# Performance work log

Hardware: AMD Instinct MI355X
Metric: run time of the kernel (lower is better)

## Reference

```python
import jax, jax.numpy as jnp
import numpy as np

N = 100000       # nodes
E = 1600000      # edges (avg degree 16)
F_IN = 20        # NUM_FEATURES
H = 128          # hidden_channels
EPS = 1e-5       # GraphNorm eps


def setup_inputs() -> dict:
    key = jax.random.key(0)
    ks = jax.random.split(key, 24)
    s = 0.05
    inp = {
        "x": jax.random.normal(ks[0], (N, F_IN), jnp.float32),
        "edge_index": jax.random.randint(ks[1], (2, E), 0, N, dtype=jnp.int32),
    }
    # SAGEConv params: lin_l (neighbors, with bias), lin_r (root, no bias)
    dims = [(F_IN, H), (H, H), (H, H)]
    k = 2
    for i, (din, dout) in enumerate(dims):
        inp[f"Wl{i}"] = jax.random.normal(ks[k], (dout, din), jnp.float32) * s; k += 1
        inp[f"bl{i}"] = jnp.zeros((dout,), jnp.float32)
        inp[f"Wr{i}"] = jax.random.normal(ks[k], (dout, din), jnp.float32) * s; k += 1
        # GraphNorm: weight, bias, mean_scale (alpha)
        inp[f"gw{i}"] = jnp.ones((dout,), jnp.float32)
        inp[f"gb{i}"] = jnp.zeros((dout,), jnp.float32)
        inp[f"ga{i}"] = jnp.ones((dout,), jnp.float32)
    # MLP head: 128 -> 64 -> 32 -> 1
    inp["hW1"] = jax.random.normal(ks[k], (64, H), jnp.float32) * s; k += 1
    inp["hb1"] = jnp.zeros((64,), jnp.float32)
    inp["hW2"] = jax.random.normal(ks[k], (32, 64), jnp.float32) * s; k += 1
    inp["hb2"] = jnp.zeros((32,), jnp.float32)
    inp["hW3"] = jax.random.normal(ks[k], (1, 32), jnp.float32) * s; k += 1
    inp["hb3"] = jnp.zeros((1,), jnp.float32)
    return inp


def _sage(x, src, dst, Wl, bl, Wr):
    # mean aggregation of source features at destination nodes
    deg = jax.ops.segment_sum(jnp.ones((src.shape[0],), x.dtype), dst, num_segments=N)
    agg = jax.ops.segment_sum(x[src], dst, num_segments=N)
    agg = agg / jnp.maximum(deg, 1.0)[:, None]
    return agg @ Wl.T + bl + x @ Wr.T


def _graphnorm(x, w, b, a):
    # single graph (batch=None): stats over all nodes, per channel
    mean = jnp.mean(x, axis=0)
    c = x - a * mean
    var = jnp.mean(c * c, axis=0)
    return w * c * jax.lax.rsqrt(var + EPS) + b


def reference(x, edge_index,
              Wl0, bl0, Wr0, gw0, gb0, ga0,
              Wl1, bl1, Wr1, gw1, gb1, ga1,
              Wl2, bl2, Wr2, gw2, gb2, ga2,
              hW1, hb1, hW2, hb2, hW3, hb3):
    src, dst = edge_index[0], edge_index[1]
    layers = [(Wl0, bl0, Wr0, gw0, gb0, ga0),
              (Wl1, bl1, Wr1, gw1, gb1, ga1),
              (Wl2, bl2, Wr2, gw2, gb2, ga2)]
    h = x
    for (Wl, bl, Wr, gw, gb, ga) in layers:
        h = _sage(h, src, dst, Wl, bl, Wr)
        h = _graphnorm(h, gw, gb, ga)
        h = jax.nn.gelu(h, approximate=False)  # dropout: eval mode (identity)
    h = jax.nn.gelu(h @ hW1.T + hb1, approximate=False)
    h = jax.nn.gelu(h @ hW2.T + hb2, approximate=False)
    out = jax.nn.sigmoid(h @ hW3.T + hb3)
    return out.squeeze(-1)  # [N]
```

## Files before the change

kernel.cpp:

```cpp
#include <hip/hip_runtime.h>
#include <hip/hip_bf16.h>
#include <math.h>

#define NN 100000
#define EE 1600000
#define FIN 20
#define HH 128
#define NBUK 391
#define FILLB 196
#define MMB 782

typedef __attribute__((ext_vector_type(8))) short bf16x8;
typedef __attribute__((ext_vector_type(4))) float f32x4;

__device__ __forceinline__ unsigned short f2b(float x) {
    unsigned int b = __float_as_uint(x);
    unsigned int r = b + 0x7fffu + ((b >> 16) & 1u);
    return (unsigned short)(r >> 16);
}
__device__ __forceinline__ float lof(unsigned int u) { return __uint_as_float(u << 16); }
__device__ __forceinline__ float hif(unsigned int u) { return __uint_as_float(u & 0xffff0000u); }

__device__ __forceinline__ float gelu_exact(float z) {
    return 0.5f * z * (1.0f + erff(z * 0.70710678118654752f));
}

__global__ __launch_bounds__(256) void kb_cnt(const int* __restrict__ dst,
                                              int* __restrict__ bcnt) {
    __shared__ int c[NBUK];
    int t = threadIdx.x;
    for (int i = t; i < NBUK; i += 256) c[i] = 0;
    __syncthreads();
    int e0 = blockIdx.x * 8192;
    #pragma unroll 4
    for (int i = 0; i < 32; ++i) {
        int e = e0 + i * 256 + t;
        if (e < EE) atomicAdd(&c[dst[e] >> 8], 1);
    }
    __syncthreads();
    for (int i = t; i < NBUK; i += 256) if (c[i]) atomicAdd(&bcnt[i], c[i]);
}

__global__ void kb_scan(const int* __restrict__ bcnt, int* __restrict__ bbase,
                        int* __restrict__ cursor) {
    __shared__ int sh[512];
    int t = threadIdx.x;
    int v = (t < NBUK) ? bcnt[t] : 0;
    sh[t] = v;
    __syncthreads();
    for (int off = 1; off < 512; off <<= 1) {
        int add = (t >= off) ? sh[t - off] : 0;
        __syncthreads();
        sh[t] += add;
        __syncthreads();
    }
    if (t < NBUK) {
        int ex = sh[t] - v;
        bbase[t] = ex;
        cursor[t] = ex;
    }
    if (t == NBUK - 1) bbase[NBUK] = sh[t];
}

__global__ __launch_bounds__(256) void kb_fill(const int* __restrict__ src,
        const int* __restrict__ dst, int* __restrict__ cursor,
        unsigned int* __restrict__ pairs) {
    __shared__ int cnt[NBUK], base[NBUK], boff[NBUK];
    int t = threadIdx.x;
    for (int i = t; i < NBUK; i += 256) { cnt[i] = 0; boff[i] = 0; }
    __syncthreads();
    int e0 = blockIdx.x * 8192;
    #pragma unroll 4
    for (int i = 0; i < 32; ++i) {
        int e = e0 + i * 256 + t;
        if (e < EE) atomicAdd(&cnt[dst[e] >> 8], 1);
    }
    __syncthreads();
    for (int i = t; i < NBUK; i += 256)
        if (cnt[i]) base[i] = atomicAdd(&cursor[i], cnt[i]);
    __syncthreads();
    #pragma unroll 4
    for (int i = 0; i < 32; ++i) {
        int e = e0 + i * 256 + t;
        if (e < EE) {
            int d = dst[e];
            int b = d >> 8;
            int pos = base[b] + atomicAdd(&boff[b], 1);
            pairs[pos] = (unsigned int)src[e] | ((unsigned int)(d & 255) << 17);
        }
    }
}

__global__ __launch_bounds__(256) void kb_csr(const unsigned int* __restrict__ pairs,
        const int* __restrict__ bbase, int* __restrict__ row_start,
        int* __restrict__ deg, float* __restrict__ invdeg, int* __restrict__ col) {
    __shared__ int ldeg[256];
    __shared__ int lcnt[256];
    int b = blockIdx.x, t = threadIdx.x;
    int e0 = bbase[b], e1 = bbase[b + 1];
    ldeg[t] = 0;
    lcnt[t] = 0;
    __syncthreads();
    for (int e = e0 + t; e < e1; e += 256) atomicAdd(&ldeg[pairs[e] >> 17], 1);
    __syncthreads();
    int d = ldeg[t];
    for (int off = 1; off < 256; off <<= 1) {
        int add = (t >= off) ? ldeg[t - off] : 0;
        __syncthreads();
        ldeg[t] += add;
        __syncthreads();
    }
    int n = b * 256 + t;
    if (n < NN) {
        row_start[n] = e0 + ldeg[t] - d;
        deg[n] = d;
        invdeg[n] = 1.0f / fmaxf((float)d, 1.0f);
    }
    __syncthreads();
    for (int e = e0 + t; e < e1; e += 256) {
        unsigned int p = pairs[e];
        int dL = p >> 17;
        int pos = e0 + (dL ? ldeg[dL - 1] : 0) + atomicAdd(&lcnt[dL], 1);
        col[pos] = (int)(p & 0x1FFFFu);
    }
}

__global__ __launch_bounds__(256) void k_packx(const float* __restrict__ x,
        unsigned short* __restrict__ A0) {
    int id = blockIdx.x * 256 + threadIdx.x;
    int n = id >> 6, k = id & 63;
    if (n >= NN) return;
    if (k < FIN) return;
    float v = (k >= 32 && k < 32 + FIN) ? x[n * FIN + (k - 32)] : 0.0f;
    A0[id] = f2b(v);
}

__global__ void k_agg0(const float* __restrict__ x, const int* __restrict__ rs,
                       const int* __restrict__ deg, const float* __restrict__ inv,
                       const int* __restrict__ col, unsigned short* __restrict__ A0) {
    int g = threadIdx.x >> 5;
    int l = threadIdx.x & 31;
    int n = blockIdx.x * 4 + g;
    if (n >= NN || l >= FIN) return;
    int s = rs[n], d = deg[n];
    float acc = 0.0f;
    int j = 0;
    for (; j + 1 < d; j += 2) {
        int c0 = col[s + j], c1 = col[s + j + 1];
        acc += x[c0 * FIN + l] + x[c1 * FIN + l];
    }
    if (j < d) acc += x[col[s + j] * FIN + l];
    A0[(size_t)n * 64 + l] = f2b(acc * inv[n]);
}

__global__ void k_pack0(const float* __restrict__ Wl, const float* __restrict__ Wr,
                        unsigned short* __restrict__ Wt) {
    int id = blockIdx.x * 256 + threadIdx.x;
    int c = id >> 6, k = id & 63;
    float v = 0.0f;
    if (k < FIN) v = Wl[c * FIN + k];
    else if (k >= 32 && k < 32 + FIN) v = Wr[c * FIN + (k - 32)];
    Wt[id] = f2b(v);
}

__global__ __launch_bounds__(64) void k_aggb(const unsigned short* __restrict__ hB,
        const int* __restrict__ rs, const int* __restrict__ deg,
        const float* __restrict__ inv, const int* __restrict__ col,
        unsigned short* __restrict__ aggB) {
    int n = blockIdx.x;
    int t = threadIdx.x;
    int s = rs[n], d = deg[n];
    const unsigned int* h32 = (const unsigned int*)hB;
    float a0 = 0.0f, a1 = 0.0f;
    int j = 0;
    for (; j + 3 < d; j += 4) {
        int c0 = col[s + j], c1 = col[s + j + 1];
        int c2 = col[s + j + 2], c3 = col[s + j + 3];
        unsigned int u0 = h32[(size_t)c0 * 64 + t];
        unsigned int u1 = h32[(size_t)c1 * 64 + t];
        unsigned int u2 = h32[(size_t)c2 * 64 + t];
        unsigned int u3 = h32[(size_t)c3 * 64 + t];
        a0 += lof(u0) + lof(u1) + lof(u2) + lof(u3);
        a1 += hif(u0) + hif(u1) + hif(u2) + hif(u3);
    }
    for (; j < d; ++j) {
        unsigned int u = h32[(size_t)col[s + j] * 64 + t];
        a0 += lof(u);
        a1 += hif(u);
    }
    float iv = inv[n];
    unsigned int o = (unsigned int)f2b(a0 * iv) | ((unsigned int)f2b(a1 * iv) << 16);
    ((unsigned int*)aggB)[(size_t)n * 64 + t] = o;
}

__global__ void k_pack_main(const float* __restrict__ Wl, const float* __restrict__ Wr,
                            unsigned short* __restrict__ Wt) {
    int id = blockIdx.x * 256 + threadIdx.x;
    int c = id >> 8, k = id & 255;
    float v = (k < HH) ? Wl[c * HH + k] : Wr[c * HH + (k - HH)];
    Wt[id] = f2b(v);
}

__global__ void k_pack_head(const float* __restrict__ hW1, const float* __restrict__ hW2,
                            const float* __restrict__ hb1, const float* __restrict__ hb2,
                            unsigned short* __restrict__ W1b, unsigned short* __restrict__ W2b,
                            float* __restrict__ bH1, float* __restrict__ bH2) {
    int id = blockIdx.x * 256 + threadIdx.x;
    if (id < 16384) {
        int c = id >> 7, k = id & 127;
        W1b[id] = f2b((c < 64) ? hW1[c * 128 + k] : 0.0f);
    } else if (id < 16384 + 2048) {
        int i = id - 16384;
        W2b[i] = f2b(hW2[i]);
    } else if (id < 16384 + 2048 + 128) {
        int i = id - 16384 - 2048;
        bH1[i] = (i < 64) ? hb1[i] : 0.0f;
    } else if (id < 16384 + 2048 + 160) {
        int i = id - 16384 - 2048 - 128;
        bH2[i] = hb2[i];
    }
}

__global__ __launch_bounds__(256) void k_mm(const unsigned short* __restrict__ A0,
        const unsigned short* __restrict__ A1, int c0, int kChunks, int lda,
        const unsigned short* __restrict__ B, int ldb,
        const float* __restrict__ bias, unsigned short* __restrict__ outB,
        float* __restrict__ psPart, float* __restrict__ pqPart, int M) {
    __shared__ __align__(16) unsigned short As[128 * 40];
    __shared__ __align__(16) unsigned short Bs[128 * 40];
    __shared__ float redS[2][128], redQ[2][128];
    const int tid = threadIdx.x;
    const int m0 = blockIdx.x * 128;
    const int w = tid >> 6, lane = tid & 63;
    const int wr = w >> 1, wc = w & 1;
    const int m16 = lane & 15, q = lane >> 4;

    f32x4 acc[4][4];
    #pragma unroll
    for (int i = 0; i < 4; ++i)
        #pragma unroll
        for (int j = 0; j < 4; ++j) acc[i][j] = (f32x4){0.f, 0.f, 0.f, 0.f};

    for (int chunk = 0; chunk < kChunks; ++chunk) {
        const unsigned short* A = (chunk < c0) ? A0 : A1;
        const int kb = (chunk - ((chunk < c0) ? 0 : c0)) * 32;
        #pragma unroll
        for (int it = 0; it < 2; ++it) {
            int s = tid + it * 256;
            int r = s >> 2, p = s & 3;
            int gm = m0 + r;
            uint4 v = make_uint4(0u, 0u, 0u, 0u);
            if (gm < M) v = *(const uint4*)(A + (size_t)gm * lda + kb + p * 8);
            *(uint4*)&As[r * 40 + p * 8] = v;
        }
        {
            const int kbB = chunk * 32;
            #pragma unroll
            for (int it = 0; it < 2; ++it) {
                int s = tid + it * 256;
                int r = s >> 2, p = s & 3;
                uint4 v = *(const uint4*)(B + (size_t)r * ldb + kbB + p * 8);
                *(uint4*)&Bs[r * 40 + p * 8] = v;
            }
        }
        __syncthreads();
        bf16x8 af[4], bfr[4];
        #pragma unroll
        for (int i = 0; i < 4; ++i)
            af[i] = *(const bf16x8*)&As[(wr * 64 + i * 16 + m16) * 40 + q * 8];
        #pragma unroll
        for (int j = 0; j < 4; ++j)
            bfr[j] = *(const bf16x8*)&Bs[(wc * 64 + j * 16 + m16) * 40 + q * 8];
        #pragma unroll
        for (int i = 0; i < 4; ++i)
            #pragma unroll
            for (int j = 0; j < 4; ++j)
                acc[i][j] = __builtin_amdgcn_mfma_f32_16x16x32_bf16(af[i], bfr[j], acc[i][j], 0, 0, 0);
        __syncthreads();
    }

    float cs[4] = {0.f, 0.f, 0.f, 0.f};
    float cq[4] = {0.f, 0.f, 0.f, 0.f};
    #pragma unroll
    for (int i = 0; i < 4; ++i) {
        int mBase = m0 + wr * 64 + i * 16 + q * 4;
        #pragma unroll
        for (int j = 0; j < 4; ++j) {
            int cc = wc * 64 + j * 16 + m16;
            float bv = bias[cc];
            #pragma unroll
            for (int r = 0; r < 4; ++r) {
                int m = mBase + r;
                float v = (m < M) ? (acc[i][j][r] + bv) : 0.0f;
                if (m < M) outB[(size_t)m * 128 + cc] = f2b(v);
                cs[j] += v;
                cq[j] += v * v;
            }
        }
    }
    #pragma unroll
    for (int msk = 16; msk < 64; msk <<= 1) {
        #pragma unroll
        for (int j = 0; j < 4; ++j) {
            cs[j] += __shfl_xor(cs[j], msk, 64);
            cq[j] += __shfl_xor(cq[j], msk, 64);
        }
    }
    if (q == 0) {
        #pragma unroll
        for (int j = 0; j < 4; ++j) {
            int cc = wc * 64 + j * 16 + m16;
            redS[wr][cc] = cs[j];
            redQ[wr][cc] = cq[j];
        }
    }
    __syncthreads();
    if (tid < 128) {
        psPart[(size_t)blockIdx.x * 128 + tid] = redS[0][tid] + redS[1][tid];
        pqPart[(size_t)blockIdx.x * 128 + tid] = redQ[0][tid] + redQ[1][tid];
    }
}

__global__ __launch_bounds__(1024) void k_gn_final(const float* __restrict__ ps,
        const float* __restrict__ pq, const float* __restrict__ gw,
        const float* __restrict__ gb, const float* __restrict__ ga,
        float* __restrict__ cA, float* __restrict__ cB, int nP) {
    __shared__ float shs[8][128], shq[8][128];
    int c = threadIdx.x & 127, sl = threadIdx.x >> 7;
    float s = 0.0f, q = 0.0f;
    for (int b = sl; b < nP; b += 8) {
        s += ps[b * 128 + c];
        q += pq[b * 128 + c];
    }
    shs[sl][c] = s;
    shq[sl][c] = q;
    __syncthreads();
    if (threadIdx.x < 128) {
        float S = 0.0f, Q = 0.0f;
        #pragma unroll
        for (int i = 0; i < 8; ++i) { S += shs[i][c]; Q += shq[i][c]; }
        float mean = S / (float)NN;
        float msq  = Q / (float)NN;
        float a = ga[c];
        float var = msq - mean * mean * a * (2.0f - a);
        float rstd = rsqrtf(var + 1e-5f);
        float A = gw[c] * rstd;
        cA[c] = A;
        cB[c] = gb[c] - a * mean * A;
    }
}

__global__ __launch_bounds__(256) void k_gn_apply(const unsigned short* __restrict__ yB,
        const float* __restrict__ cA, const float* __restrict__ cB,
        unsigned short* __restrict__ hB) {
    int i = blockIdx.x * 256 + threadIdx.x;
    if (i >= NN * 16) return;
    int g = i & 15;
    uint4 v = ((const uint4*)yB)[i];
    float4 A0 = ((const float4*)cA)[g * 2];
    float4 A1 = ((const float4*)cA)[g * 2 + 1];
    float4 B0 = ((const float4*)cB)[g * 2];
    float4 B1 = ((const float4*)cB)[g * 2 + 1];
    unsigned int o0 = (unsigned int)f2b(gelu_exact(lof(v.x) * A0.x + B0.x))
                    | ((unsigned int)f2b(gelu_exact(hif(v.x) * A0.y + B0.y)) << 16);
    unsigned int o1 = (unsigned int)f2b(gelu_exact(lof(v.y) * A0.z + B0.z))
                    | ((unsigned int)f2b(gelu_exact(hif(v.y) * A0.w + B0.w)) << 16);
    unsigned int o2 = (unsigned int)f2b(gelu_exact(lof(v.z) * A1.x + B1.x))
                    | ((unsigned int)f2b(gelu_exact(hif(v.z) * A1.y + B1.y)) << 16);
    unsigned int o3 = (unsigned int)f2b(gelu_exact(lof(v.w) * A1.z + B1.z))
                    | ((unsigned int)f2b(gelu_exact(hif(v.w) * A1.w + B1.w)) << 16);
    ((uint4*)hB)[i] = make_uint4(o0, o1, o2, o3);
}

__global__ __launch_bounds__(256) void k_headf(const unsigned short* __restrict__ hB,
        const unsigned short* __restrict__ W1b, const float* __restrict__ b1,
        const unsigned short* __restrict__ W2b, const float* __restrict__ b2,
        const float* __restrict__ W3, const float* __restrict__ b3,
        float* __restrict__ out) {
    __shared__ __align__(16) unsigned short As[128 * 40];
    __shared__ __align__(16) unsigned short Bs[128 * 40];
    __shared__ __align__(16) unsigned short As2[128 * 72];
    __shared__ __align__(16) unsigned short Bs2[32 * 72];
    const int tid = threadIdx.x;
    const int m0 = blockIdx.x * 128;
    const int w = tid >> 6, lane = tid & 63;
    const int wr = w >> 1, wc = w & 1;
    const int m16 = lane & 15, q = lane >> 4;

    f32x4 acc1[4][4];
    #pragma unroll
    for (int i = 0; i < 4; ++i)
        #pragma unroll
        for (int j = 0; j < 4; ++j) acc1[i][j] = (f32x4){0.f, 0.f, 0.f, 0.f};

    for (int chunk = 0; chunk < 4; ++chunk) {
        const int kb = chunk * 32;
        #pragma unroll
        for (int it = 0; it < 2; ++it) {
            int s = tid + it * 256;
            int r = s >> 2, p = s & 3;
            int gm = m0 + r;
            uint4 v = make_uint4(0u, 0u, 0u, 0u);
            if (gm < NN) v = *(const uint4*)(hB + (size_t)gm * 128 + kb + p * 8);
            *(uint4*)&As[r * 40 + p * 8] = v;
        }
        #pragma unroll
        for (int it = 0; it < 2; ++it) {
            int s = tid + it * 256;
            int r = s >> 2, p = s & 3;
            uint4 v = *(const uint4*)(W1b + (size_t)r * 128 + kb + p * 8);
            *(uint4*)&Bs[r * 40 + p * 8] = v;
        }
        __syncthreads();
        bf16x8 af[4], bfr[4];
        #pragma unroll
        for (int i = 0; i < 4; ++i)
            af[i] = *(const bf16x8*)&As[(wr * 64 + i * 16 + m16) * 40 + q * 8];
        #pragma unroll
        for (int j = 0; j < 4; ++j)
            bfr[j] = *(const bf16x8*)&Bs[(wc * 64 + j * 16 + m16) * 40 + q * 8];
        #pragma unroll
        for (int i = 0; i < 4; ++i)
            #pragma unroll
            for (int j = 0; j < 4; ++j)
                acc1[i][j] = __builtin_amdgcn_mfma_f32_16x16x32_bf16(af[i], bfr[j], acc1[i][j], 0, 0, 0);
        __syncthreads();
    }

    #pragma unroll
    for (int it = 0; it < 8; ++it) {
        int i = tid + it * 256;
        if (i < 2048) Bs2[(i >> 6) * 72 + (i & 63)] = W2b[i];
    }
    if (wc == 0) {
        float b1v[4];
        #pragma unroll
        for (int j = 0; j < 4; ++j) b1v[j] = b1[j * 16 + m16];
        #pragma unroll
        for (int i = 0; i < 4; ++i) {
            int mloc = wr * 64 + i * 16 + q * 4;
            #pragma unroll
            for (int j = 0; j < 4; ++j) {
                int c = j * 16 + m16;
                #pragma unroll
                for (int r = 0; r < 4; ++r)
                    As2[(mloc + r) * 72 + c] = f2b(gelu_exact(acc1[i][j][r] + b1v[j]));
            }
        }
    }
    __syncthreads();

    f32x4 acc2[2][2];
    #pragma unroll
    for (int i = 0; i < 2; ++i)
        #pragma unroll
        for (int j = 0; j < 2; ++j) acc2[i][j] = (f32x4){0.f, 0.f, 0.f, 0.f};
    #pragma unroll
    for (int kc = 0; kc < 2; ++kc) {
        bf16x8 a2[2], bf2[2];
        #pragma unroll
        for (int i = 0; i < 2; ++i)
            a2[i] = *(const bf16x8*)&As2[(w * 32 + i * 16 + m16) * 72 + kc * 32 + q * 8];
        #pragma unroll
        for (int j = 0; j < 2; ++j)
            bf2[j] = *(const bf16x8*)&Bs2[(j * 16 + m16) * 72 + kc * 32 + q * 8];
        #pragma unroll
        for (int i = 0; i < 2; ++i)
            #pragma unroll
            for (int j = 0; j < 2; ++j)
                acc2[i][j] = __builtin_amdgcn_mfma_f32_16x16x32_bf16(a2[i], bf2[j], acc2[i][j], 0, 0, 0);
    }

    float w3a = W3[m16], w3b = W3[16 + m16];
    float b2a = b2[m16], b2b = b2[16 + m16];
    float p[8];
    #pragma unroll
    for (int i = 0; i < 2; ++i)
        #pragma unroll
        for (int r = 0; r < 4; ++r) {
            float za = gelu_exact(acc2[i][0][r] + b2a);
            float zb = gelu_exact(acc2[i][1][r] + b2b);
            p[i * 4 + r] = za * w3a + zb * w3b;
        }
    #pragma unroll
    for (int msk = 1; msk < 16; msk <<= 1)
        #pragma unroll
        for (int k = 0; k < 8; ++k) p[k] += __shfl_xor(p[k], msk, 64);
    if (m16 == 0) {
        float b3v = b3[0];
        #pragma unroll
        for (int i = 0; i < 2; ++i)
            #pragma unroll
            for (int r = 0; r < 4; ++r) {
                int m = m0 + w * 32 + i * 16 + q * 4 + r;
                if (m < NN) out[m] = 1.0f / (1.0f + expf(-(p[i * 4 + r] + b3v)));
            }
    }
}

extern "C" void kernel_launch(void* const* d_in, const int* in_sizes, int n_in,
                              void* d_out, int out_size, void* d_ws, size_t ws_size,
                              hipStream_t stream) {
    const float* x   = (const float*)d_in[0];
    const int*   ei  = (const int*)d_in[1];
    const float* Wl0 = (const float*)d_in[2];
    const float* bl0 = (const float*)d_in[3];
    const float* Wr0 = (const float*)d_in[4];
    const float* gw0 = (const float*)d_in[5];
    const float* gb0 = (const float*)d_in[6];
    const float* ga0 = (const float*)d_in[7];
    const float* Wl1 = (const float*)d_in[8];
    const float* bl1 = (const float*)d_in[9];
    const float* Wr1 = (const float*)d_in[10];
    const float* gw1 = (const float*)d_in[11];
    const float* gb1 = (const float*)d_in[12];
    const float* ga1 = (const float*)d_in[13];
    const float* Wl2 = (const float*)d_in[14];
    const float* bl2 = (const float*)d_in[15];
    const float* Wr2 = (const float*)d_in[16];
    const float* gw2 = (const float*)d_in[17];
    const float* gb2 = (const float*)d_in[18];
    const float* ga2 = (const float*)d_in[19];
    const float* hW1 = (const float*)d_in[20];
    const float* hb1 = (const float*)d_in[21];
    const float* hW2 = (const float*)d_in[22];
    const float* hb2 = (const float*)d_in[23];
    const float* hW3 = (const float*)d_in[24];
    const float* hb3 = (const float*)d_in[25];
    float* out = (float*)d_out;

    size_t off = 0;
    auto carve = [&](size_t bytes) -> void* {
        void* p = (void*)((char*)d_ws + off);
        off += (bytes + 255) & ~(size_t)255;
        return p;
    };
    int*   bcnt      = (int*)carve((size_t)NBUK * 4);
    int*   bbase     = (int*)carve((size_t)(NBUK + 1) * 4);
    int*   cursor    = (int*)carve((size_t)NBUK * 4);
    unsigned int* pairs = (unsigned int*)carve((size_t)EE * 4);
    int*   deg       = (int*)carve((size_t)NN * 4);
    int*   row_start = (int*)carve((size_t)NN * 4);
    float* invdeg    = (float*)carve((size_t)NN * 4);
    int*   colarr    = (int*)carve((size_t)EE * 4);
    unsigned short* Wt0   = (unsigned short*)carve(128 * 64 * 2);
    unsigned short* Wt2   = (unsigned short*)carve(128 * 256 * 2);
    unsigned short* W1b   = (unsigned short*)carve(128 * 128 * 2);
    unsigned short* W2b   = (unsigned short*)carve(32 * 64 * 2);
    float* biasH1    = (float*)carve(128 * 4);
    float* biasH2    = (float*)carve(32 * 4);
    float* ps        = (float*)carve((size_t)MMB * 128 * 4);
    float* pq        = (float*)carve((size_t)MMB * 128 * 4);
    float* coefA     = (float*)carve(128 * 4);
    float* coefB     = (float*)carve(128 * 4);
    unsigned short* A0pack = (unsigned short*)carve((size_t)NN * 64 * 2);
    unsigned short* hB   = (unsigned short*)carve((size_t)NN * HH * 2);
    unsigned short* aggB = (unsigned short*)carve((size_t)NN * HH * 2);
    unsigned short* yB   = (unsigned short*)carve((size_t)NN * HH * 2);
    if (off > ws_size) return;

    const int* src = ei;
    const int* dst = ei + EE;

    hipMemsetAsync(bcnt, 0, (size_t)NBUK * 4, stream);
    kb_cnt<<<FILLB, 256, 0, stream>>>(dst, bcnt);
    kb_scan<<<1, 512, 0, stream>>>(bcnt, bbase, cursor);
    kb_fill<<<FILLB, 256, 0, stream>>>(src, dst, cursor, pairs);
    kb_csr<<<NBUK, 256, 0, stream>>>(pairs, bbase, row_start, deg, invdeg, colarr);

    k_packx<<<(NN * 64 + 255) / 256, 256, 0, stream>>>(x, A0pack);
    k_agg0<<<(NN + 3) / 4, 128, 0, stream>>>(x, row_start, deg, invdeg, colarr, A0pack);
    k_pack0<<<32, 256, 0, stream>>>(Wl0, Wr0, Wt0);
    k_mm<<<MMB, 256, 0, stream>>>(A0pack, A0pack, 2, 2, 64, Wt0, 64, bl0, yB, ps, pq, NN);
    k_gn_final<<<1, 1024, 0, stream>>>(ps, pq, gw0, gb0, ga0, coefA, coefB, MMB);
    k_gn_apply<<<(NN * 16 + 255) / 256, 256, 0, stream>>>(yB, coefA, coefB, hB);

    const float* WlL[2] = {Wl1, Wl2};
    const float* blL[2] = {bl1, bl2};
    const float* WrL[2] = {Wr1, Wr2};
    const float* gwL[2] = {gw1, gw2};
    const float* gbL[2] = {gb1, gb2};
    const float* gaL[2] = {ga1, ga2};
    for (int l = 0; l < 2; ++l) {
        k_pack_main<<<128, 256, 0, stream>>>(WlL[l], WrL[l], Wt2);
        k_aggb<<<NN, 64, 0, stream>>>(hB, row_start, deg, invdeg, colarr, aggB);
        k_mm<<<MMB, 256, 0, stream>>>(aggB, hB, 4, 8, 128, Wt2, 256, blL[l],
                                      yB, ps, pq, NN);
        k_gn_final<<<1, 1024, 0, stream>>>(ps, pq, gwL[l], gbL[l], gaL[l], coefA, coefB, MMB);
        k_gn_apply<<<(NN * 16 + 255) / 256, 256, 0, stream>>>(yB, coefA, coefB, hB);
    }

    k_pack_head<<<(16384 + 2048 + 160 + 255) / 256, 256, 0, stream>>>(
        hW1, hW2, hb1, hb2, W1b, W2b, biasH1, biasH2);
    k_headf<<<MMB, 256, 0, stream>>>(hB, W1b, biasH1, W2b, biasH2, hW3, hb3, out);
}
```

Before: 598.5 us.

## Aggregate layer-0 from bf16-packed x and trim head GEMM to 64 outputs

Adds a pre-pass that packs x into a 32-wide bf16 row layout. Layer-0 neighbour aggregation then gathers two features per 32-bit load using 16 threads per node and 16 nodes per block, which cuts gather traffic and idle lanes. The head kernel no longer pads the first MLP layer to 128 outputs: each wave computes 32 rows by 64 columns, shared memory is aliased into one pool, and the W2 tile is loaded up front. The cost is an extra packing kernel and bf16 rounding of x before aggregation, where the sum was previously taken in fp32 over the original values.

```diff
diff --git a/kernel.cpp b/kernel.cpp
--- a/kernel.cpp
+++ b/kernel.cpp
@@ -125,6 +125,14 @@
     }
 }
 
+__global__ __launch_bounds__(256) void k_packxb(const float* __restrict__ x,
+        unsigned short* __restrict__ xb) {
+    int id = blockIdx.x * 256 + threadIdx.x;
+    if (id >= NN * 32) return;
+    int n = id >> 5, k = id & 31;
+    xb[id] = f2b((k < FIN) ? x[n * FIN + k] : 0.0f);
+}
+
 __global__ __launch_bounds__(256) void k_packx(const float* __restrict__ x,
         unsigned short* __restrict__ A0) {
     int id = blockIdx.x * 256 + threadIdx.x;
@@ -135,22 +143,34 @@
     A0[id] = f2b(v);
 }
 
-__global__ void k_agg0(const float* __restrict__ x, const int* __restrict__ rs,
-                       const int* __restrict__ deg, const float* __restrict__ inv,
-                       const int* __restrict__ col, unsigned short* __restrict__ A0) {
-    int g = threadIdx.x >> 5;
-    int l = threadIdx.x & 31;
-    int n = blockIdx.x * 4 + g;
-    if (n >= NN || l >= FIN) return;
+__global__ __launch_bounds__(256) void k_agg0(const unsigned int* __restrict__ xb32,
+        const int* __restrict__ rs, const int* __restrict__ deg,
+        const float* __restrict__ inv, const int* __restrict__ col,
+        unsigned short* __restrict__ A0) {
+    int g = threadIdx.x >> 4;
+    int l = threadIdx.x & 15;
+    int n = blockIdx.x * 16 + g;
+    if (n >= NN) return;
     int s = rs[n], d = deg[n];
-    float acc = 0.0f;
+    float a0 = 0.0f, a1 = 0.0f;
     int j = 0;
     for (; j + 1 < d; j += 2) {
         int c0 = col[s + j], c1 = col[s + j + 1];
-        acc += x[c0 * FIN + l] + x[c1 * FIN + l];
-    }
-    if (j < d) acc += x[col[s + j] * FIN + l];
-    A0[(size_t)n * 64 + l] = f2b(acc * inv[n]);
+        unsigned int u0 = xb32[c0 * 16 + l];
+        unsigned int u1 = xb32[c1 * 16 + l];
+        a0 += lof(u0) + lof(u1);
+        a1 += hif(u0) + hif(u1);
+    }
+    if (j < d) {
+        unsigned int u = xb32[col[s + j] * 16 + l];
+        a0 += lof(u);
+        a1 += hif(u);
+    }
+    if (l < 10) {
+        float iv = inv[n];
+        unsigned int o = (unsigned int)f2b(a0 * iv) | ((unsigned int)f2b(a1 * iv) << 16);
+        ((unsigned int*)A0)[(size_t)n * 32 + l] = o;
+    }
 }
 
 __global__ void k_pack0(const float* __restrict__ Wl, const float* __restrict__ Wr,
@@ -206,18 +226,14 @@
                             unsigned short* __restrict__ W1b, unsigned short* __restrict__ W2b,
                             float* __restrict__ bH1, float* __restrict__ bH2) {
     int id = blockIdx.x * 256 + threadIdx.x;
-    if (id < 16384) {
-        int c = id >> 7, k = id & 127;
-        W1b[id] = f2b((c < 64) ? hW1[c * 128 + k] : 0.0f);
-    } else if (id < 16384 + 2048) {
-        int i = id - 16384;
-        W2b[i] = f2b(hW2[i]);
-    } else if (id < 16384 + 2048 + 128) {
-        int i = id - 16384 - 2048;
-        bH1[i] = (i < 64) ? hb1[i] : 0.0f;
-    } else if (id < 16384 + 2048 + 160) {
-        int i = id - 16384 - 2048 - 128;
-        bH2[i] = hb2[i];
+    if (id < 8192) {
+        W1b[id] = f2b(hW1[id]);
+    } else if (id < 8192 + 2048) {
+        W2b[id - 8192] = f2b(hW2[id - 8192]);
+    } else if (id < 8192 + 2048 + 64) {
+        bH1[id - 8192 - 2048] = hb1[id - 8192 - 2048];
+    } else if (id < 8192 + 2048 + 96) {
+        bH2[id - 8192 - 2048 - 64] = hb2[id - 8192 - 2048 - 64];
     }
 }
 
@@ -377,19 +393,25 @@
         const unsigned short* __restrict__ W2b, const float* __restrict__ b2,
         const float* __restrict__ W3, const float* __restrict__ b3,
         float* __restrict__ out) {
-    __shared__ __align__(16) unsigned short As[128 * 40];
-    __shared__ __align__(16) unsigned short Bs[128 * 40];
-    __shared__ __align__(16) unsigned short As2[128 * 72];
-    __shared__ __align__(16) unsigned short Bs2[32 * 72];
+    __shared__ __align__(16) char pool[23040];
+    unsigned short* As  = (unsigned short*)pool;
+    unsigned short* Bs  = (unsigned short*)(pool + 10240);
+    unsigned short* As2 = (unsigned short*)pool;
+    unsigned short* Bs2 = (unsigned short*)(pool + 18432);
     const int tid = threadIdx.x;
     const int m0 = blockIdx.x * 128;
     const int w = tid >> 6, lane = tid & 63;
-    const int wr = w >> 1, wc = w & 1;
     const int m16 = lane & 15, q = lane >> 4;
 
-    f32x4 acc1[4][4];
-    #pragma unroll
-    for (int i = 0; i < 4; ++i)
+    #pragma unroll
+    for (int it = 0; it < 8; ++it) {
+        int i = tid + it * 256;
+        if (i < 2048) Bs2[(i >> 6) * 72 + (i & 63)] = W2b[i];
+    }
+
+    f32x4 acc1[2][4];
+    #pragma unroll
+    for (int i = 0; i < 2; ++i)
         #pragma unroll
         for (int j = 0; j < 4; ++j) acc1[i][j] = (f32x4){0.f, 0.f, 0.f, 0.f};
 
@@ -404,41 +426,34 @@
             if (gm < NN) v = *(const uint4*)(hB + (size_t)gm * 128 + kb + p * 8);
             *(uint4*)&As[r * 40 + p * 8] = v;
         }
-        #pragma unroll
-        for (int it = 0; it < 2; ++it) {
-            int s = tid + it * 256;
-            int r = s >> 2, p = s & 3;
+        {
+            int r = tid >> 2, p = tid & 3;
             uint4 v = *(const uint4*)(W1b + (size_t)r * 128 + kb + p * 8);
             *(uint4*)&Bs[r * 40 + p * 8] = v;
         }
         __syncthreads();
-        bf16x8 af[4], bfr[4];
-        #pragma unroll
-        for (int i = 0; i < 4; ++i)
-            af[i] = *(const bf16x8*)&As[(wr * 64 + i * 16 + m16) * 40 + q * 8];
+        bf16x8 af[2], bfr[4];
+        #pragma unroll
+        for (int i = 0; i < 2; ++i)
+            af[i] = *(const bf16x8*)&As[(w * 32 + i * 16 + m16) * 40 + q * 8];
         #pragma unroll
         for (int j = 0; j < 4; ++j)
-            bfr[j] = *(const bf16x8*)&Bs[(wc * 64 + j * 16 + m16) * 40 + q * 8];
-        #pragma unroll
-        for (int i = 0; i < 4; ++i)
+            bfr[j] = *(const bf16x8*)&Bs[(j * 16 + m16) * 40 + q * 8];
+        #pragma unroll
+        for (int i = 0; i < 2; ++i)
             #pragma unroll
             for (int j = 0; j < 4; ++j)
                 acc1[i][j] = __builtin_amdgcn_mfma_f32_16x16x32_bf16(af[i], bfr[j], acc1[i][j], 0, 0, 0);
         __syncthreads();
     }
 
-    #pragma unroll
-    for (int it = 0; it < 8; ++it) {
-        int i = tid + it * 256;
-        if (i < 2048) Bs2[(i >> 6) * 72 + (i & 63)] = W2b[i];
-    }
-    if (wc == 0) {
+    {
         float b1v[4];
         #pragma unroll
         for (int j = 0; j < 4; ++j) b1v[j] = b1[j * 16 + m16];
         #pragma unroll
-        for (int i = 0; i < 4; ++i) {
-            int mloc = wr * 64 + i * 16 + q * 4;
+        for (int i = 0; i < 2; ++i) {
+            int mloc = w * 32 + i * 16 + q * 4;
             #pragma unroll
             for (int j = 0; j < 4; ++j) {
                 int c = j * 16 + m16;
@@ -543,11 +558,12 @@
     int*   row_start = (int*)carve((size_t)NN * 4);
     float* invdeg    = (float*)carve((size_t)NN * 4);
     int*   colarr    = (int*)carve((size_t)EE * 4);
+    unsigned short* xb    = (unsigned short*)carve((size_t)NN * 32 * 2);
     unsigned short* Wt0   = (unsigned short*)carve(128 * 64 * 2);
     unsigned short* Wt2   = (unsigned short*)carve(128 * 256 * 2);
-    unsigned short* W1b   = (unsigned short*)carve(128 * 128 * 2);
+    unsigned short* W1b   = (unsigned short*)carve(64 * 128 * 2);
     unsigned short* W2b   = (unsigned short*)carve(32 * 64 * 2);
-    float* biasH1    = (float*)carve(128 * 4);
+    float* biasH1    = (float*)carve(64 * 4);
     float* biasH2    = (float*)carve(32 * 4);
     float* ps        = (float*)carve((size_t)MMB * 128 * 4);
     float* pq        = (float*)carve((size_t)MMB * 128 * 4);
@@ -568,8 +584,10 @@
     kb_fill<<<FILLB, 256, 0, stream>>>(src, dst, cursor, pairs);
     kb_csr<<<NBUK, 256, 0, stream>>>(pairs, bbase, row_start, deg, invdeg, colarr);
 
+    k_packxb<<<(NN * 32 + 255) / 256, 256, 0, stream>>>(x, xb);
     k_packx<<<(NN * 64 + 255) / 256, 256, 0, stream>>>(x, A0pack);
-    k_agg0<<<(NN + 3) / 4, 128, 0, stream>>>(x, row_start, deg, invdeg, colarr, A0pack);
+    k_agg0<<<(NN + 15) / 16, 256, 0, stream>>>((const unsigned int*)xb, row_start,
+                                               deg, invdeg, colarr, A0pack);
     k_pack0<<<32, 256, 0, stream>>>(Wl0, Wr0, Wt0);
     k_mm<<<MMB, 256, 0, stream>>>(A0pack, A0pack, 2, 2, 64, Wt0, 64, bl0, yB, ps, pq, NN);
     k_gn_final<<<1, 1024, 0, stream>>>(ps, pq, gw0, gb0, ga0, coefA, coefB, MMB);
@@ -590,7 +608,7 @@
         k_gn_apply<<<(NN * 16 + 255) / 256, 256, 0, stream>>>(yB, coefA, coefB, hB);
     }
 
-    k_pack_head<<<(16384 + 2048 + 160 + 255) / 256, 256, 0, stream>>>(
+    k_pack_head<<<(8192 + 2048 + 96 + 255) / 256, 256, 0, stream>>>(
         hW1, hW2, hb1, hb2, W1b, W2b, biasH1, biasH2);
     k_headf<<<MMB, 256, 0, stream>>>(hB, W1b, biasH1, W2b, biasH2, hW3, hb3, out);
 }
```

Measured after the change: 562.9 us. -5.9%, faster.
